# Performance work log

Measured on AMD Instinct MI355X. Metric: run time of the kernel, lower is better.

Reference implementation:

```python
import jax, jax.numpy as jnp
import numpy as np

DIM, C_HID, N_HEADS = 128, 32, 4
INF = 1.0e9
LN_EPS = 1e-5


def setup_inputs() -> dict:
    key = jax.random.key(0)
    ks = jax.random.split(key, 10)
    B, I, J, C, H, D = 1, 256, 256, DIM, N_HEADS, C_HID
    s = 0.02
    return {
        "x": jax.random.normal(ks[0], (B, I, J, C), jnp.float32),
        "mask": jnp.ones((B, I, J), jnp.float32),
        "ln_w": jnp.ones((C,), jnp.float32),
        "ln_b": jnp.zeros((C,), jnp.float32),
        "tri_w": jax.random.normal(ks[1], (C, H), jnp.float32) * s,  # bias=False
        "q_w": jax.random.normal(ks[2], (C, H * D), jnp.float32) * s,
        "k_w": jax.random.normal(ks[3], (C, H * D), jnp.float32) * s,
        "v_w": jax.random.normal(ks[4], (C, H * D), jnp.float32) * s,
        "g_w": jax.random.normal(ks[5], (C, H * D), jnp.float32) * s,
        "g_b": jnp.ones((H * D,), jnp.float32),  # gating init: bias=1
        "o_w": jax.random.normal(ks[6], (H * D, C), jnp.float32) * s,
        "o_b": jnp.zeros((C,), jnp.float32),
    }


def _layer_norm(x, w, b):
    mu = jnp.mean(x, axis=-1, keepdims=True)
    var = jnp.mean(jnp.square(x - mu), axis=-1, keepdims=True)
    return (x - mu) * jax.lax.rsqrt(var + LN_EPS) * w + b


def reference(x, mask, ln_w, ln_b, tri_w, q_w, k_w, v_w, g_w, g_b, o_w, o_b):
    # starting=True: no transpose. x: [B, I, J, C], mask: [B, I, J]
    B, I, J, C = x.shape
    H, D = N_HEADS, C_HID
    xn = _layer_norm(x, ln_w, ln_b)

    # mask bias: [B, I, 1, 1, J]; triangle bias: [B, 1, H, I(J), J]
    mask_bias = (INF * (mask - 1.0))[:, :, None, None, :]
    tri_bias = jnp.einsum("bijc,ch->bhij", xn, tri_w)[:, None]

    def proj(w):  # [B, I, H, J, D]
        return (xn @ w).reshape(B, I, J, H, D).transpose(0, 1, 3, 2, 4)

    q = proj(q_w) * (D ** -0.5)
    k = proj(k_w)
    v = proj(v_w)

    logits = jnp.einsum("bihqd,bihkd->bihqk", q, k) + mask_bias + tri_bias
    a = jax.nn.softmax(logits, axis=-1)
    o = jnp.einsum("bihqk,bihkd->bihqd", a, v).transpose(0, 1, 3, 2, 4)  # [B,I,J,H,D]

    g = jax.nn.sigmoid(xn @ g_w + g_b).reshape(B, I, J, H, D)
    o = (o * g).reshape(B, I, J, H * D)
    return o @ o_w + o_b
```

## Files before the change

kernel.cpp:

```cpp
#include <hip/hip_runtime.h>
#include <hip/hip_bf16.h>
#include <math.h>

#define LOG2E_ 1.4426950408889634f

typedef short short8 __attribute__((ext_vector_type(8)));
typedef float f32x4 __attribute__((ext_vector_type(4)));
typedef int int4v __attribute__((ext_vector_type(4)));

#if defined(__has_builtin)
#if __has_builtin(__builtin_amdgcn_exp2f)
#define EXP2F(x) __builtin_amdgcn_exp2f(x)
#else
#define EXP2F(x) exp2f(x)
#endif
#else
#define EXP2F(x) exp2f(x)
#endif

static __device__ __forceinline__ unsigned short f2bf(float f) {
    union { float f; unsigned int u; } c; c.f = f;
    c.u += 0x7fffu + ((c.u >> 16) & 1u);
    return (unsigned short)(c.u >> 16);
}
static __device__ __forceinline__ int pk2bf(float a, float b) {
    union { __hip_bfloat162 h; int i; } u;
    u.h = __float22bfloat162_rn(make_float2(a, b));
    return u.i;
}

__global__ __launch_bounds__(256) void ln_prep_kernel(
    const float* __restrict__ x, const float* __restrict__ ln_w,
    const float* __restrict__ ln_b, const float* __restrict__ tri_w,
    const float* __restrict__ qw, const float* __restrict__ kw,
    const float* __restrict__ vw, const float* __restrict__ gw,
    const float* __restrict__ ow,
    unsigned short* __restrict__ xn, unsigned short* __restrict__ triT,
    unsigned short* __restrict__ wt)
{
    const int bid = blockIdx.x, tid = threadIdx.x;
    if (bid >= 8192) {
        int id = (bid - 8192) * 256 + tid;
        int wsel = id >> 14;
        int e = id & 16383;
        int kk = e >> 7, n = e & 127;
        const float* src = (wsel == 0) ? qw : (wsel == 1) ? kw : (wsel == 2) ? vw
                         : (wsel == 3) ? gw : ow;
        float scale = (wsel == 0) ? (0.17677669529663687f * LOG2E_) : 1.0f;
        wt[wsel * 16384 + n * 128 + kk] = f2bf(src[kk * 128 + n] * scale);
        return;
    }

    const int row = bid * 8 + (tid >> 5);
    const int l = tid & 31;

    float4 xv = *(const float4*)(x + (size_t)row * 128 + l * 4);
    float s = (xv.x + xv.y) + (xv.z + xv.w);
    #pragma unroll
    for (int mk = 16; mk >= 1; mk >>= 1) s += __shfl_xor(s, mk, 64);
    float mu = s * (1.0f / 128.0f);

    float d0 = xv.x - mu, d1 = xv.y - mu, d2 = xv.z - mu, d3 = xv.w - mu;
    float sq = (d0 * d0 + d1 * d1) + (d2 * d2 + d3 * d3);
    #pragma unroll
    for (int mk = 16; mk >= 1; mk >>= 1) sq += __shfl_xor(sq, mk, 64);
    float rstd = rsqrtf(sq * (1.0f / 128.0f) + 1e-5f);

    float4 wv = *(const float4*)(ln_w + l * 4);
    float4 bv = *(const float4*)(ln_b + l * 4);
    float n0 = d0 * rstd * wv.x + bv.x;
    float n1 = d1 * rstd * wv.y + bv.y;
    float n2 = d2 * rstd * wv.z + bv.z;
    float n3 = d3 * rstd * wv.w + bv.w;

    ushort4 xo;
    xo.x = f2bf(n0); xo.y = f2bf(n1); xo.z = f2bf(n2); xo.w = f2bf(n3);
    *(ushort4*)(xn + (size_t)row * 128 + l * 4) = xo;

    float4 t0 = *(const float4*)(tri_w + (l * 4 + 0) * 4);
    float4 t1 = *(const float4*)(tri_w + (l * 4 + 1) * 4);
    float4 t2 = *(const float4*)(tri_w + (l * 4 + 2) * 4);
    float4 t3 = *(const float4*)(tri_w + (l * 4 + 3) * 4);
    float ax = (n0 * t0.x + n1 * t1.x) + (n2 * t2.x + n3 * t3.x);
    float ay = (n0 * t0.y + n1 * t1.y) + (n2 * t2.y + n3 * t3.y);
    float az = (n0 * t0.z + n1 * t1.z) + (n2 * t2.z + n3 * t3.z);
    float aw = (n0 * t0.w + n1 * t1.w) + (n2 * t2.w + n3 * t3.w);
    #pragma unroll
    for (int mk = 16; mk >= 1; mk >>= 1) {
        ax += __shfl_xor(ax, mk, 64);
        ay += __shfl_xor(ay, mk, 64);
        az += __shfl_xor(az, mk, 64);
        aw += __shfl_xor(aw, mk, 64);
    }
    if (l < 4) {
        float v = (l == 0) ? ax : (l == 1) ? ay : (l == 2) ? az : aw;
        int q = row >> 8, kc = row & 255;
        int off = l * 65536 + (q >> 4) * 4096 + (kc >> 4) * 256
                + (q & 15) * 16 + (kc & 15);
        triT[off] = f2bf(v * LOG2E_);
    }
}

__global__ __launch_bounds__(1024, 4) void mega_kernel(
    const unsigned short* __restrict__ xn, const unsigned short* __restrict__ wt,
    const float* __restrict__ g_b, const float* __restrict__ mask,
    const unsigned short* __restrict__ triT, const float* __restrict__ o_b,
    float* __restrict__ out)
{
    __shared__ __align__(16) char WBUF[2 * 43008];
    __shared__ __align__(16) unsigned short Qg[256 * 40];
    __shared__ __align__(16) unsigned short Kl[256 * 40];
    __shared__ __align__(16) unsigned short Vc[32 * 264];
    __shared__ float mb[256];

    const int i = blockIdx.x;
    const int tid = threadIdx.x;
    const int w = tid >> 6, lane = tid & 63, g = lane >> 4, m = lane & 15;
    const f32x4 zero = {0.f, 0.f, 0.f, 0.f};

    short8 xa[4];
    #pragma unroll
    for (int kc = 0; kc < 4; ++kc)
        xa[kc] = *(const short8*)(xn + (size_t)(i * 256 + w * 16 + m) * 128
                                  + kc * 32 + 8 * g);
    if (tid < 256) mb[tid] = (mask[i * 256 + tid] - 1.0f) * (1.0e9f * LOG2E_);

    #pragma unroll
    for (int it = 0; it < 3; ++it) {
        int gi = it * 1024 + tid;
        if (gi < 2048) {
            int sl = gi >> 9, e = gi & 511, row = e >> 4, c8 = e & 15;
            short8 v = *(const short8*)(wt + sl * 16384 + row * 128 + c8 * 8);
            *(short8*)(WBUF + sl * 8192 +
                       ((row * 256 + c8 * 16) ^ ((row & 7) << 4))) = v;
        } else if (gi < 2560) {
            int go = gi - 2048, n = go >> 2, k8 = go & 3;
            short8 v = *(const short8*)(wt + 65536 + n * 128 + k8 * 8);
            *(short8*)(WBUF + 32768 + n * 80 + k8 * 16) = v;
        }
    }
    __syncthreads();

    const int srcA = ((g & 1) << 1) | (g >> 1);
    const int idxA = (srcA * 16 + m) * 4;
    const int idxB = idxA ^ 64;
    const bool low = (lane < 32);
    const bool odd = (g & 1);
    const char* VcB0 = (const char*)Vc + m * 528;
    const char* VcB1 = (const char*)Vc + (16 + m) * 528;

    f32x4 oacc[8];
    #pragma unroll
    for (int nt = 0; nt < 8; ++nt) oacc[nt] = zero;

    const int qrow = w * 16 + m;

    #pragma unroll 1
    for (int h = 0; h < 4; ++h) {
        const char* wb = WBUF + (h & 1) * 43008;

        {
            f32x4 aq[2] = {zero, zero}, ak[2] = {zero, zero};
            #pragma unroll
            for (int kc = 0; kc < 4; ++kc) {
                short8 b0[2], b1[2];
                #pragma unroll
                for (int nt = 0; nt < 2; ++nt) {
                    int row = nt * 16 + m;
                    int off = (row * 256 + kc * 64 + 16 * g) ^ ((row & 7) << 4);
                    b0[nt] = *(const short8*)(wb + off);
                    b1[nt] = *(const short8*)(wb + 8192 + off);
                }
                #pragma unroll
                for (int nt = 0; nt < 2; ++nt) {
                    aq[nt] = __builtin_amdgcn_mfma_f32_16x16x32_bf16(b0[nt], xa[kc], aq[nt], 0, 0, 0);
                    ak[nt] = __builtin_amdgcn_mfma_f32_16x16x32_bf16(b1[nt], xa[kc], ak[nt], 0, 0, 0);
                }
            }
            #pragma unroll
            for (int nt = 0; nt < 2; ++nt) {
                int col = nt * 16 + 4 * g;
                ushort4 q4, k4;
                q4.x = f2bf(aq[nt][0]); q4.y = f2bf(aq[nt][1]);
                q4.z = f2bf(aq[nt][2]); q4.w = f2bf(aq[nt][3]);
                k4.x = f2bf(ak[nt][0]); k4.y = f2bf(ak[nt][1]);
                k4.z = f2bf(ak[nt][2]); k4.w = f2bf(ak[nt][3]);
                *(ushort4*)(Qg + qrow * 40 + col) = q4;
                *(ushort4*)(Kl + qrow * 40 + col) = k4;
            }
        }

        f32x4 gacc[2];
        {
            f32x4 av4[2] = {zero, zero}, ag[2] = {zero, zero};
            #pragma unroll
            for (int kc = 0; kc < 4; ++kc) {
                short8 b0[2], b1[2];
                #pragma unroll
                for (int nt = 0; nt < 2; ++nt) {
                    int row = nt * 16 + m;
                    int off = (row * 256 + kc * 64 + 16 * g) ^ ((row & 7) << 4);
                    b0[nt] = *(const short8*)(wb + 16384 + off);
                    b1[nt] = *(const short8*)(wb + 24576 + off);
                }
                #pragma unroll
                for (int nt = 0; nt < 2; ++nt) {
                    av4[nt] = __builtin_amdgcn_mfma_f32_16x16x32_bf16(b0[nt], xa[kc], av4[nt], 0, 0, 0);
                    ag[nt]  = __builtin_amdgcn_mfma_f32_16x16x32_bf16(b1[nt], xa[kc], ag[nt], 0, 0, 0);
                }
            }
            #pragma unroll
            for (int nt = 0; nt < 2; ++nt) {
                int col = nt * 16 + 4 * g;
                #pragma unroll
                for (int r = 0; r < 4; ++r) {
                    Vc[(col + r) * 264 + qrow] = f2bf(av4[nt][r]);
                    gacc[nt][r] = 1.0f / (1.0f + __expf(-(ag[nt][r] + g_b[h * 32 + col + r])));
                }
            }
        }

        short8 sv0, sv1, sv2;
        if (h < 3) {
            int hh = h + 1;
            { int sl = tid >> 9, e = tid & 511, row = e >> 4, c8 = e & 15;
              sv0 = *(const short8*)(wt + sl * 16384 + (hh * 32 + row) * 128 + c8 * 8); }
            { int gi = 1024 + tid; int sl = gi >> 9, e = gi & 511, row = e >> 4, c8 = e & 15;
              sv1 = *(const short8*)(wt + sl * 16384 + (hh * 32 + row) * 128 + c8 * 8); }
            if (tid < 512) { int n = tid >> 2, k8 = tid & 3;
              sv2 = *(const short8*)(wt + 65536 + n * 128 + hh * 32 + k8 * 8); }
        }
        __syncthreads();

        const short8 qf = *(const short8*)((const char*)Qg + qrow * 80 + 16 * g);
        const unsigned short* triQ = triT + h * 65536 + w * 4096 + m * 16 + 4 * g;

        float ls = 0.f;
        f32x4 o0 = zero, o1 = zero;

        #pragma unroll
        for (int c = 0; c < 8; ++c) {
            int d00, d01, d10, d11;
            {
                const int kt = 2 * c;
                short8 af = *(const short8*)((const char*)Kl + (kt * 16 + m) * 80 + 16 * g);
                f32x4 acc = __builtin_amdgcn_mfma_f32_16x16x32_bf16(af, qf, zero, 0, 0, 0);
                f32x4 mbv = *(const f32x4*)(mb + kt * 16 + 4 * g);
                int2 td = *(const int2*)(triQ + kt * 256);
                float t0 = __uint_as_float((unsigned)td.x << 16);
                float t1 = __uint_as_float((unsigned)td.x & 0xffff0000u);
                float t2 = __uint_as_float((unsigned)td.y << 16);
                float t3 = __uint_as_float((unsigned)td.y & 0xffff0000u);
                float p0 = EXP2F(acc[0] + mbv[0] + t0);
                float p1 = EXP2F(acc[1] + mbv[1] + t1);
                float p2 = EXP2F(acc[2] + mbv[2] + t2);
                float p3 = EXP2F(acc[3] + mbv[3] + t3);
                ls += (p0 + p1) + (p2 + p3);
                d00 = pk2bf(p0, p1); d01 = pk2bf(p2, p3);
            }
            {
                const int kt = 2 * c + 1;
                short8 af = *(const short8*)((const char*)Kl + (kt * 16 + m) * 80 + 16 * g);
                f32x4 acc = __builtin_amdgcn_mfma_f32_16x16x32_bf16(af, qf, zero, 0, 0, 0);
                f32x4 mbv = *(const f32x4*)(mb + kt * 16 + 4 * g);
                int2 td = *(const int2*)(triQ + kt * 256);
                float t0 = __uint_as_float((unsigned)td.x << 16);
                float t1 = __uint_as_float((unsigned)td.x & 0xffff0000u);
                float t2 = __uint_as_float((unsigned)td.y << 16);
                float t3 = __uint_as_float((unsigned)td.y & 0xffff0000u);
                float p0 = EXP2F(acc[0] + mbv[0] + t0);
                float p1 = EXP2F(acc[1] + mbv[1] + t1);
                float p2 = EXP2F(acc[2] + mbv[2] + t2);
                float p3 = EXP2F(acc[3] + mbv[3] + t3);
                ls += (p0 + p1) + (p2 + p3);
                d10 = pk2bf(p0, p1); d11 = pk2bf(p2, p3);
            }
            int pk0 = odd ? d10 : d00;
            int pk1 = odd ? d11 : d01;
            int pk2 = odd ? d00 : d10;
            int pk3 = odd ? d01 : d11;

            int dA0 = __builtin_amdgcn_ds_bpermute(idxA, pk0);
            int dA1 = __builtin_amdgcn_ds_bpermute(idxA, pk1);
            int dB0 = __builtin_amdgcn_ds_bpermute(idxB, pk2);
            int dB1 = __builtin_amdgcn_ds_bpermute(idxB, pk3);
            int4v bi;
            bi.x = low ? dA0 : dB0;
            bi.y = low ? dA1 : dB1;
            bi.z = low ? dB0 : dA0;
            bi.w = low ? dB1 : dA1;
            short8 bs = __builtin_bit_cast(short8, bi);

            short8 av0 = *(const short8*)(VcB0 + c * 64 + 16 * g);
            short8 av1 = *(const short8*)(VcB1 + c * 64 + 16 * g);
            o0 = __builtin_amdgcn_mfma_f32_16x16x32_bf16(av0, bs, o0, 0, 0, 0);
            o1 = __builtin_amdgcn_mfma_f32_16x16x32_bf16(av1, bs, o1, 0, 0, 0);
        }
        ls += __shfl_xor(ls, 16, 64);
        ls += __shfl_xor(ls, 32, 64);
        float inv = 1.0f / ls;

        ushort4 s0, s1;
        s0.x = f2bf(o0[0] * inv * gacc[0][0]);
        s0.y = f2bf(o0[1] * inv * gacc[0][1]);
        s0.z = f2bf(o0[2] * inv * gacc[0][2]);
        s0.w = f2bf(o0[3] * inv * gacc[0][3]);
        s1.x = f2bf(o1[0] * inv * gacc[1][0]);
        s1.y = f2bf(o1[1] * inv * gacc[1][1]);
        s1.z = f2bf(o1[2] * inv * gacc[1][2]);
        s1.w = f2bf(o1[3] * inv * gacc[1][3]);
        *(ushort4*)(Qg + qrow * 40 + 4 * g) = s0;
        *(ushort4*)(Qg + qrow * 40 + 16 + 4 * g) = s1;

        if (h < 3) {
            char* db = WBUF + ((h + 1) & 1) * 43008;
            { int sl = tid >> 9, e = tid & 511, row = e >> 4, c8 = e & 15;
              *(short8*)(db + sl * 8192 +
                         ((row * 256 + c8 * 16) ^ ((row & 7) << 4))) = sv0; }
            { int gi = 1024 + tid; int sl = gi >> 9, e = gi & 511, row = e >> 4, c8 = e & 15;
              *(short8*)(db + sl * 8192 +
                         ((row * 256 + c8 * 16) ^ ((row & 7) << 4))) = sv1; }
            if (tid < 512) { int n = tid >> 2, k8 = tid & 3;
              *(short8*)(db + 32768 + n * 80 + k8 * 16) = sv2; }
        }

        {
            short8 a = *(const short8*)((const char*)Qg + qrow * 80 + 16 * g);
            #pragma unroll
            for (int nt = 0; nt < 8; ++nt) {
                short8 b = *(const short8*)(wb + 32768 + (nt * 16 + m) * 80 + 16 * g);
                oacc[nt] = __builtin_amdgcn_mfma_f32_16x16x32_bf16(b, a, oacc[nt], 0, 0, 0);
            }
        }
        __syncthreads();
    }

    const int orow = i * 256 + qrow;
    #pragma unroll
    for (int nt = 0; nt < 8; ++nt) {
        int col = nt * 16 + 4 * g;
        float4 bv = *(const float4*)(o_b + col);
        float4 o;
        o.x = oacc[nt][0] + bv.x;
        o.y = oacc[nt][1] + bv.y;
        o.z = oacc[nt][2] + bv.z;
        o.w = oacc[nt][3] + bv.w;
        *(float4*)(out + (size_t)orow * 128 + col) = o;
    }
}

extern "C" void kernel_launch(void* const* d_in, const int* in_sizes, int n_in,
                              void* d_out, int out_size, void* d_ws, size_t ws_size,
                              hipStream_t stream) {
    (void)in_sizes; (void)n_in; (void)out_size; (void)ws_size;
    const float* x    = (const float*)d_in[0];
    const float* mask = (const float*)d_in[1];
    const float* ln_w = (const float*)d_in[2];
    const float* ln_b = (const float*)d_in[3];
    const float* tri_w= (const float*)d_in[4];
    const float* q_w  = (const float*)d_in[5];
    const float* k_w  = (const float*)d_in[6];
    const float* v_w  = (const float*)d_in[7];
    const float* g_w  = (const float*)d_in[8];
    const float* g_b  = (const float*)d_in[9];
    const float* o_w  = (const float*)d_in[10];
    const float* o_b  = (const float*)d_in[11];

    char* ws = (char*)d_ws;
    unsigned short* xn  = (unsigned short*)(ws);
    unsigned short* tri = (unsigned short*)(ws + 16777216);
    unsigned short* wt  = (unsigned short*)(ws + 17301504);

    ln_prep_kernel<<<8512, 256, 0, stream>>>(x, ln_w, ln_b, tri_w,
                                             q_w, k_w, v_w, g_w, o_w,
                                             xn, tri, wt);
    mega_kernel<<<256, 1024, 0, stream>>>(xn, wt, g_b, mask, tri, o_b,
                                          (float*)d_out);
}
```

Before: 75.54 us.

## Pre-swizzle per-head weight images and stream them to LDS via global_load_lds

```diff
diff --git a/kernel.cpp b/kernel.cpp
--- a/kernel.cpp
+++ b/kernel.cpp
@@ -28,6 +28,11 @@
     u.h = __float22bfloat162_rn(make_float2(a, b));
     return u.i;
 }
+static __device__ __forceinline__ void load_lds16(const void* g, void* l) {
+    __builtin_amdgcn_global_load_lds(
+        (const __attribute__((address_space(1))) void*)g,
+        (__attribute__((address_space(3))) void*)l, 16, 0, 0);
+}
 
 __global__ __launch_bounds__(256) void ln_prep_kernel(
     const float* __restrict__ x, const float* __restrict__ ln_w,
@@ -36,18 +41,39 @@
     const float* __restrict__ vw, const float* __restrict__ gw,
     const float* __restrict__ ow,
     unsigned short* __restrict__ xn, unsigned short* __restrict__ triT,
-    unsigned short* __restrict__ wt)
+    char* __restrict__ wimg)
 {
     const int bid = blockIdx.x, tid = threadIdx.x;
     if (bid >= 8192) {
         int id = (bid - 8192) * 256 + tid;
-        int wsel = id >> 14;
-        int e = id & 16383;
-        int kk = e >> 7, n = e & 127;
-        const float* src = (wsel == 0) ? qw : (wsel == 1) ? kw : (wsel == 2) ? vw
-                         : (wsel == 3) ? gw : ow;
-        float scale = (wsel == 0) ? (0.17677669529663687f * LOG2E_) : 1.0f;
-        wt[wsel * 16384 + n * 128 + kk] = f2bf(src[kk * 128 + n] * scale);
+        int h = id / 2688;
+        int b = (id - h * 2688) * 16;
+        unsigned short v[8];
+        if (b < 32768) {
+            int sl = b >> 13;
+            int bi = b & 8191;
+            int row = bi >> 8;
+            int c8 = ((bi >> 4) & 15) ^ (row & 7);
+            const float* src = (sl == 0) ? qw : (sl == 1) ? kw : (sl == 2) ? vw : gw;
+            float scale = (sl == 0) ? (0.17677669529663687f * LOG2E_) : 1.0f;
+            int R = h * 32 + row;
+            #pragma unroll
+            for (int e = 0; e < 8; ++e)
+                v[e] = f2bf(src[(c8 * 8 + e) * 128 + R] * scale);
+        } else {
+            int o = b - 32768;
+            int n = o / 80;
+            int k8 = (o - n * 80) >> 4;
+            if (k8 < 4) {
+                #pragma unroll
+                for (int e = 0; e < 8; ++e)
+                    v[e] = f2bf(ow[(h * 32 + k8 * 8 + e) * 128 + n]);
+            } else {
+                #pragma unroll
+                for (int e = 0; e < 8; ++e) v[e] = 0;
+            }
+        }
+        *(short8*)(wimg + h * 43008 + b) = *(short8*)v;
         return;
     }
 
@@ -102,7 +128,7 @@
 }
 
 __global__ __launch_bounds__(1024, 4) void mega_kernel(
-    const unsigned short* __restrict__ xn, const unsigned short* __restrict__ wt,
+    const unsigned short* __restrict__ xn, const char* __restrict__ wimg,
     const float* __restrict__ g_b, const float* __restrict__ mask,
     const unsigned short* __restrict__ triT, const float* __restrict__ o_b,
     float* __restrict__ out)
@@ -125,19 +151,12 @@
                                   + kc * 32 + 8 * g);
     if (tid < 256) mb[tid] = (mask[i * 256 + tid] - 1.0f) * (1.0e9f * LOG2E_);
 
-    #pragma unroll
-    for (int it = 0; it < 3; ++it) {
-        int gi = it * 1024 + tid;
-        if (gi < 2048) {
-            int sl = gi >> 9, e = gi & 511, row = e >> 4, c8 = e & 15;
-            short8 v = *(const short8*)(wt + sl * 16384 + row * 128 + c8 * 8);
-            *(short8*)(WBUF + sl * 8192 +
-                       ((row * 256 + c8 * 16) ^ ((row & 7) << 4))) = v;
-        } else if (gi < 2560) {
-            int go = gi - 2048, n = go >> 2, k8 = go & 3;
-            short8 v = *(const short8*)(wt + 65536 + n * 128 + k8 * 8);
-            *(short8*)(WBUF + 32768 + n * 80 + k8 * 16) = v;
-        }
+    {
+        const char* src = wimg + w * 1024 + lane * 16;
+        char* dst = WBUF + w * 1024;
+        load_lds16(src, dst);
+        load_lds16(src + 16384, dst + 16384);
+        if (w < 10) load_lds16(src + 32768, dst + 32768);
     }
     __syncthreads();
 
@@ -190,47 +209,38 @@
             }
         }
 
-        f32x4 gacc[2];
         {
-            f32x4 av4[2] = {zero, zero}, ag[2] = {zero, zero};
+            f32x4 av4[2] = {zero, zero};
             #pragma unroll
             for (int kc = 0; kc < 4; ++kc) {
-                short8 b0[2], b1[2];
+                short8 b0[2];
                 #pragma unroll
                 for (int nt = 0; nt < 2; ++nt) {
                     int row = nt * 16 + m;
                     int off = (row * 256 + kc * 64 + 16 * g) ^ ((row & 7) << 4);
                     b0[nt] = *(const short8*)(wb + 16384 + off);
-                    b1[nt] = *(const short8*)(wb + 24576 + off);
                 }
                 #pragma unroll
-                for (int nt = 0; nt < 2; ++nt) {
+                for (int nt = 0; nt < 2; ++nt)
                     av4[nt] = __builtin_amdgcn_mfma_f32_16x16x32_bf16(b0[nt], xa[kc], av4[nt], 0, 0, 0);
-                    ag[nt]  = __builtin_amdgcn_mfma_f32_16x16x32_bf16(b1[nt], xa[kc], ag[nt], 0, 0, 0);
-                }
             }
             #pragma unroll
             for (int nt = 0; nt < 2; ++nt) {
                 int col = nt * 16 + 4 * g;
                 #pragma unroll
-                for (int r = 0; r < 4; ++r) {
+                for (int r = 0; r < 4; ++r)
                     Vc[(col + r) * 264 + qrow] = f2bf(av4[nt][r]);
-                    gacc[nt][r] = 1.0f / (1.0f + __expf(-(ag[nt][r] + g_b[h * 32 + col + r])));
-                }
-            }
-        }
-
-        short8 sv0, sv1, sv2;
+            }
+        }
+        __syncthreads();
+
         if (h < 3) {
-            int hh = h + 1;
-            { int sl = tid >> 9, e = tid & 511, row = e >> 4, c8 = e & 15;
-              sv0 = *(const short8*)(wt + sl * 16384 + (hh * 32 + row) * 128 + c8 * 8); }
-            { int gi = 1024 + tid; int sl = gi >> 9, e = gi & 511, row = e >> 4, c8 = e & 15;
-              sv1 = *(const short8*)(wt + sl * 16384 + (hh * 32 + row) * 128 + c8 * 8); }
-            if (tid < 512) { int n = tid >> 2, k8 = tid & 3;
-              sv2 = *(const short8*)(wt + 65536 + n * 128 + hh * 32 + k8 * 8); }
-        }
-        __syncthreads();
+            const char* src = wimg + (h + 1) * 43008 + w * 1024 + lane * 16;
+            char* dst = WBUF + ((h + 1) & 1) * 43008 + w * 1024;
+            load_lds16(src, dst);
+            load_lds16(src + 16384, dst + 16384);
+            if (w < 10) load_lds16(src + 32768, dst + 32768);
+        }
 
         const short8 qf = *(const short8*)((const char*)Qg + qrow * 80 + 16 * g);
         const unsigned short* triQ = triT + h * 65536 + w * 4096 + m * 16 + 4 * g;
@@ -300,28 +310,34 @@
         ls += __shfl_xor(ls, 32, 64);
         float inv = 1.0f / ls;
 
-        ushort4 s0, s1;
-        s0.x = f2bf(o0[0] * inv * gacc[0][0]);
-        s0.y = f2bf(o0[1] * inv * gacc[0][1]);
-        s0.z = f2bf(o0[2] * inv * gacc[0][2]);
-        s0.w = f2bf(o0[3] * inv * gacc[0][3]);
-        s1.x = f2bf(o1[0] * inv * gacc[1][0]);
-        s1.y = f2bf(o1[1] * inv * gacc[1][1]);
-        s1.z = f2bf(o1[2] * inv * gacc[1][2]);
-        s1.w = f2bf(o1[3] * inv * gacc[1][3]);
-        *(ushort4*)(Qg + qrow * 40 + 4 * g) = s0;
-        *(ushort4*)(Qg + qrow * 40 + 16 + 4 * g) = s1;
-
-        if (h < 3) {
-            char* db = WBUF + ((h + 1) & 1) * 43008;
-            { int sl = tid >> 9, e = tid & 511, row = e >> 4, c8 = e & 15;
-              *(short8*)(db + sl * 8192 +
-                         ((row * 256 + c8 * 16) ^ ((row & 7) << 4))) = sv0; }
-            { int gi = 1024 + tid; int sl = gi >> 9, e = gi & 511, row = e >> 4, c8 = e & 15;
-              *(short8*)(db + sl * 8192 +
-                         ((row * 256 + c8 * 16) ^ ((row & 7) << 4))) = sv1; }
-            if (tid < 512) { int n = tid >> 2, k8 = tid & 3;
-              *(short8*)(db + 32768 + n * 80 + k8 * 16) = sv2; }
+        {
+            f32x4 ag[2] = {zero, zero};
+            #pragma unroll
+            for (int kc = 0; kc < 4; ++kc) {
+                short8 b1[2];
+                #pragma unroll
+                for (int nt = 0; nt < 2; ++nt) {
+                    int row = nt * 16 + m;
+                    int off = (row * 256 + kc * 64 + 16 * g) ^ ((row & 7) << 4);
+                    b1[nt] = *(const short8*)(wb + 24576 + off);
+                }
+                #pragma unroll
+                for (int nt = 0; nt < 2; ++nt)
+                    ag[nt] = __builtin_amdgcn_mfma_f32_16x16x32_bf16(b1[nt], xa[kc], ag[nt], 0, 0, 0);
+            }
+            float4 gb0 = *(const float4*)(g_b + h * 32 + 4 * g);
+            float4 gb1 = *(const float4*)(g_b + h * 32 + 16 + 4 * g);
+            ushort4 s0, s1;
+            s0.x = f2bf(o0[0] * inv / (1.0f + __expf(-(ag[0][0] + gb0.x))));
+            s0.y = f2bf(o0[1] * inv / (1.0f + __expf(-(ag[0][1] + gb0.y))));
+            s0.z = f2bf(o0[2] * inv / (1.0f + __expf(-(ag[0][2] + gb0.z))));
+            s0.w = f2bf(o0[3] * inv / (1.0f + __expf(-(ag[0][3] + gb0.w))));
+            s1.x = f2bf(o1[0] * inv / (1.0f + __expf(-(ag[1][0] + gb1.x))));
+            s1.y = f2bf(o1[1] * inv / (1.0f + __expf(-(ag[1][1] + gb1.y))));
+            s1.z = f2bf(o1[2] * inv / (1.0f + __expf(-(ag[1][2] + gb1.z))));
+            s1.w = f2bf(o1[3] * inv / (1.0f + __expf(-(ag[1][3] + gb1.w))));
+            *(ushort4*)(Qg + qrow * 40 + 4 * g) = s0;
+            *(ushort4*)(Qg + qrow * 40 + 16 + 4 * g) = s1;
         }
 
         {
@@ -369,11 +385,11 @@
     char* ws = (char*)d_ws;
     unsigned short* xn  = (unsigned short*)(ws);
     unsigned short* tri = (unsigned short*)(ws + 16777216);
-    unsigned short* wt  = (unsigned short*)(ws + 17301504);
-
-    ln_prep_kernel<<<8512, 256, 0, stream>>>(x, ln_w, ln_b, tri_w,
+    char*           wimg= (char*)(ws + 17301504);
+
+    ln_prep_kernel<<<8234, 256, 0, stream>>>(x, ln_w, ln_b, tri_w,
                                              q_w, k_w, v_w, g_w, o_w,
-                                             xn, tri, wt);
-    mega_kernel<<<256, 1024, 0, stream>>>(xn, wt, g_b, mask, tri, o_b,
+                                             xn, tri, wimg);
+    mega_kernel<<<256, 1024, 0, stream>>>(xn, wimg, g_b, mask, tri, o_b,
                                           (float*)d_out);
 }
```

Result: slower. 98.64 us (+30.6%).
